# Kernel tuning notes

Measured on AMD Instinct MI355X. Metric: run time of the kernel, lower is better.

## Reference

```python
import jax, jax.numpy as jnp
import numpy as np

L, D, H, HK, DH, F, V, T, B = 8, 1024, 16, 4, 64, 2816, 32000, 1024, 2
G = H // HK
THETA = 10000.0
EPS = 1e-6
SCALE = DH ** -0.5


def _rope_tables(t, dh, theta):
    inv = 1.0 / theta ** (jnp.arange(0, dh, 2, dtype=jnp.float32) / dh)  # [dh/2]
    ang = jnp.arange(t, dtype=jnp.float32)[:, None] * inv[None, :]       # [T, dh/2]
    return jnp.cos(ang), jnp.sin(ang)


def _apply_rope(x, cos, sin):
    # x: [B, T, h, DH] -> rotate pairs (even, odd)
    xr = x.reshape(*x.shape[:-1], DH // 2, 2)
    x0, x1 = xr[..., 0], xr[..., 1]
    c = cos[None, :, None, :]
    s = sin[None, :, None, :]
    out = jnp.stack([x0 * c - x1 * s, x0 * s + x1 * c], axis=-1)
    return out.reshape(*x.shape)


def _rmsnorm(x, w):
    var = jnp.mean(x * x, axis=-1, keepdims=True)
    return x * jax.lax.rsqrt(var + EPS) * w


def setup_inputs() -> dict:
    key = jax.random.key(0)
    ks = jax.random.split(key, 10)
    s = 0.02
    return {
        "ids": jax.random.randint(ks[0], (B, T), 0, V),
        "emb": jax.random.normal(ks[1], (V, D), jnp.float32) * s,
        "qw": jax.random.normal(ks[2], (L, H * DH, D), jnp.float32) * s,
        "kw": jax.random.normal(ks[3], (L, HK * DH, D), jnp.float32) * s,
        "vw": jax.random.normal(ks[4], (L, HK * DH, D), jnp.float32) * s,
        "ow": jax.random.normal(ks[5], (L, D, D), jnp.float32) * s,
        "w1": jax.random.normal(ks[6], (L, F, D), jnp.float32) * s,
        "w2": jax.random.normal(ks[7], (L, D, F), jnp.float32) * s,
        "w3": jax.random.normal(ks[8], (L, F, D), jnp.float32) * s,
        "n1": jnp.ones((L, D), jnp.float32),
        "n2": jnp.ones((L, D), jnp.float32),
        "nf": jnp.ones((D,), jnp.float32),
    }


def _forward(ids, emb, qw, kw, vw, ow, w1, w2, w3, n1, n2, nf):
    cos, sin = _rope_tables(T, DH, THETA)
    causal = jnp.tril(jnp.ones((T, T), dtype=bool))  # [T, T]
    x = emb[ids]  # [B, T, D]
    for l in range(L):
        xn = _rmsnorm(x, n1[l])
        q = jnp.einsum("btd,ed->bte", xn, qw[l]).reshape(B, T, H, DH)
        k = jnp.einsum("btd,ed->bte", xn, kw[l]).reshape(B, T, HK, DH)
        v = jnp.einsum("btd,ed->bte", xn, vw[l]).reshape(B, T, HK, DH)
        q = _apply_rope(q, cos, sin)
        k = _apply_rope(k, cos, sin)
        # GQA: group query heads over shared kv heads
        qg = q.transpose(0, 2, 1, 3).reshape(B, HK, G, T, DH)
        kh = k.transpose(0, 2, 1, 3)  # [B, HK, T, DH]
        vh = v.transpose(0, 2, 1, 3)
        scores = jnp.einsum("bkgtd,bksd->bkgts", qg, kh) * SCALE
        scores = jnp.where(causal, scores, -jnp.inf)
        p = jax.nn.softmax(scores, axis=-1)
        out = jnp.einsum("bkgts,bksd->bkgtd", p, vh)
        out = out.reshape(B, H, T, DH).transpose(0, 2, 1, 3).reshape(B, T, D)
        x = x + jnp.einsum("btd,ed->bte", out, ow[l])
        xn2 = _rmsnorm(x, n2[l])
        h1 = jnp.einsum("btd,fd->btf", xn2, w1[l])
        h3 = jnp.einsum("btd,fd->btf", xn2, w3[l])
        x = x + jnp.einsum("btf,df->btd", jax.nn.silu(h1) * h3, w2[l])
    x = _rmsnorm(x, nf)
    logits = jnp.einsum("btd,vd->btv", x, emb)  # tied lm_head
    return logits


def reference(ids, emb, qw, kw, vw, ow, w1, w2, w3, n1, n2, nf):
    return _forward(ids, emb, qw, kw, vw, ow, w1, w2, w3, n1, n2, nf)
```

## Files before the change

kernel.cpp:

```cpp
#include <hip/hip_runtime.h>
#include <math.h>

#define L_ 8
#define D_ 1024
#define H_ 16
#define HK_ 4
#define DH_ 64
#define F_ 2816
#define V_ 32000
#define T_ 1024
#define B_ 2
#define M_ (B_*T_)
#define SCALE_ 0.125f

typedef unsigned short u16;
typedef unsigned int   u32;
typedef __attribute__((ext_vector_type(4))) float  f32x4;
typedef __attribute__((ext_vector_type(8))) short  bf16x8;
typedef __attribute__((ext_vector_type(4))) unsigned short u16x4;
typedef __attribute__((ext_vector_type(4))) unsigned int   u32x4;

__device__ __forceinline__ float bf2f(u16 h) {
    union { u32 u; float f; } v; v.u = ((u32)h) << 16; return v.f;
}
__device__ __forceinline__ u16 f2bf(float f) {
    union { float f; u32 u; } v; v.f = f;
    u32 r = v.u + 0x7fffu + ((v.u >> 16) & 1u);
    return (u16)(r >> 16);
}

__device__ __forceinline__ void gl_lds16(const void* g, void* l) {
    __builtin_amdgcn_global_load_lds(
        (const __attribute__((address_space(1))) unsigned int*)g,
        (__attribute__((address_space(3))) unsigned int*)l,
        16, 0, 0);
}

__device__ __forceinline__ void bar8() {
    asm volatile("" ::: "memory");
    __builtin_amdgcn_s_barrier();
    asm volatile("" ::: "memory");
}

template<int EPI>
__global__ __launch_bounds__(512)
void gemm8_k(const u16* __restrict__ A, int K,
             const u16* __restrict__ W, int N,
             float* __restrict__ Of, u16* __restrict__ Ob)
{
    constexpr int TS = 256 * 64;
    __shared__ u16 sA[2 * TS];
    __shared__ u16 sB[2 * TS];

    const int tid = threadIdx.x;
    const int lane = tid & 63, wv = tid >> 6;
    const int wm = wv >> 2, wn = wv & 3;
    const int l15 = lane & 15, lhi = lane >> 4;

    const int nwg = gridDim.x;
    const int q8 = nwg >> 3;
    const int xcd = blockIdx.x & 7, off8 = blockIdx.x >> 3;
    const int wgid = xcd * q8 + off8;
    const int tM = wgid & 7, tN = wgid >> 3;

    const u16* Abase = A + (size_t)(tM * 256) * K;
    const u16* Wbase = W + (size_t)(tN * 256) * K;

    const int srow8 = lane >> 3;
    const int sp    = lane & 7;
    const int scol  = (sp ^ srow8) * 8;

    auto stage = [&](const u16* gbase, int t2, int h, u16* dst) {
        const u16* g = gbase + (size_t)(h * 128) * K + (t2 << 6);
        u16* d = dst + h * 8192;
#pragma unroll
        for (int i = 0; i < 2; ++i) {
            int c = wv * 2 + i;
            int row = c * 8 + srow8;
            gl_lds16(g + (size_t)row * K + scol, d + c * 512);
        }
    };

    f32x4 acc[8][4];
#pragma unroll
    for (int i = 0; i < 8; ++i)
#pragma unroll
        for (int j = 0; j < 4; ++j) acc[i][j] = f32x4{0.f, 0.f, 0.f, 0.f};

    const int nt = K >> 6;
    stage(Abase, 0, 0, sA); stage(Abase, 0, 1, sA);
    stage(Wbase, 0, 0, sB); stage(Wbase, 0, 1, sB);
    if (nt > 1) {
        stage(Wbase, 1, 0, sB + TS); stage(Wbase, 1, 1, sB + TS);
        asm volatile("s_waitcnt vmcnt(4)" ::: "memory");
    } else {
        asm volatile("s_waitcnt vmcnt(0)" ::: "memory");
    }
    bar8();

    for (int t = 0; t < nt; ++t) {
        const int cur = t & 1;
        const u16* sa = sA + cur * TS;
        const u16* sb = sB + cur * TS;
        u16* saN = sA + (cur ^ 1) * TS;
        u16* sbN = sB + cur * TS;

        bf16x8 breg[4][2];

#pragma unroll
        for (int p = 0; p < 4; ++p) {
            if (p == 0) {
#pragma unroll
                for (int j = 0; j < 4; ++j)
#pragma unroll
                    for (int kk = 0; kk < 2; ++kk) {
                        int br = wn * 64 + j * 16 + l15;
                        int ls = kk * 4 + lhi;
                        breg[j][kk] = *(const bf16x8*)
                            &sb[br * 64 + ((ls ^ (br & 7)) * 8)];
                    }
            }
            bf16x8 areg[2][2];
#pragma unroll
            for (int mi = 0; mi < 2; ++mi)
#pragma unroll
                for (int kk = 0; kk < 2; ++kk) {
                    int ar = wm * 128 + (p * 2 + mi) * 16 + l15;
                    int ls = kk * 4 + lhi;
                    areg[mi][kk] = *(const bf16x8*)
                        &sa[ar * 64 + ((ls ^ (ar & 7)) * 8)];
                }

            if (p == 0 && t + 1 < nt) stage(Abase, t + 1, 0, saN);
            if (p == 1 && t + 1 < nt) stage(Abase, t + 1, 1, saN);
            if (p == 2 && t + 2 < nt) stage(Wbase, t + 2, 0, sbN);
            if (p == 3 && t + 2 < nt) stage(Wbase, t + 2, 1, sbN);

            if (p == 3 && t + 1 < nt) {
                if (t + 2 < nt) asm volatile("s_waitcnt vmcnt(4)" ::: "memory");
                else            asm volatile("s_waitcnt vmcnt(0)" ::: "memory");
            }

            bar8();
            asm volatile("s_waitcnt lgkmcnt(0)" ::: "memory");
            __builtin_amdgcn_s_setprio(1);
#pragma unroll
            for (int mi = 0; mi < 2; ++mi)
#pragma unroll
                for (int j = 0; j < 4; ++j)
#pragma unroll
                    for (int kk = 0; kk < 2; ++kk)
                        acc[p * 2 + mi][j] = __builtin_amdgcn_mfma_f32_16x16x32_bf16(
                            areg[mi][kk], breg[j][kk], acc[p * 2 + mi][j], 0, 0, 0);
            __builtin_amdgcn_s_setprio(0);
            bar8();
        }
    }

    if (EPI == 1) {
        float* sw = (float*)sA + wv * (16 * 68);
        const int cc = l15;
#pragma unroll
        for (int i = 0; i < 8; ++i) {
#pragma unroll
            for (int j = 0; j < 4; ++j)
#pragma unroll
                for (int r = 0; r < 4; ++r)
                    sw[(lhi * 4 + r) * 68 + j * 16 + l15] = acc[i][j][r];
#pragma unroll
            for (int g = 0; g < 4; ++g) {
                int row = g * 4 + lhi;
                f32x4 v = *(const f32x4*)&sw[row * 68 + cc * 4];
                size_t gm = (size_t)tM * 256 + wm * 128 + i * 16 + row;
                size_t gn = (size_t)tN * 256 + wn * 64 + cc * 4;
                *(f32x4*)&Of[gm * (size_t)N + gn] = v;
            }
        }
    } else {
#pragma unroll
        for (int i = 0; i < 8; ++i)
#pragma unroll
            for (int j = 0; j < 4; ++j) {
                size_t gm = (size_t)tM * 256 + wm * 128 + i * 16 + lhi * 4;
                size_t gn = (size_t)tN * 256 + wn * 64 + j * 16 + l15;
#pragma unroll
                for (int r = 0; r < 4; ++r) {
                    float v = acc[i][j][r];
                    float b = __shfl_xor(v, 1);
                    if ((lane & 1) == 0) {
                        float s = v / (1.0f + expf(-v));
                        Ob[(gm + r) * (size_t)F_ + (gn >> 1)] = f2bf(s * b);
                    }
                }
            }
    }
}

template<int BM, int BN, int EPI>
__global__ __launch_bounds__(256)
void gemm2_k(const u16* __restrict__ A, int K,
             const u16* __restrict__ W, int N,
             float* __restrict__ Of, u16* __restrict__ Ob,
             const float* __restrict__ tc, const float* __restrict__ ts)
{
    constexpr int FM = BM / 32;
    constexpr int FN = BN / 32;
    constexpr int GM = M_ / BM;
    constexpr int IPA = BM / 64;
    constexpr int IPB = BN / 64;
    __shared__ u16 sA[2 * BM * 32];
    __shared__ u16 sB[2 * BN * 32];

    const int tid  = threadIdx.x;
    const int lane = tid & 63, wv = tid >> 6;
    const int wm = wv >> 1, wn = wv & 1;
    const int l15 = lane & 15, lhi = lane >> 4;
    const int m0 = wm * (BM / 2), n0 = wn * (BN / 2);

    const int nwg = gridDim.x;
    const int q8 = nwg >> 3, r8 = nwg & 7;
    const int xcd = blockIdx.x & 7, off8 = blockIdx.x >> 3;
    const int wgid = (xcd < r8 ? xcd * (q8 + 1) : r8 * (q8 + 1) + (xcd - r8) * q8) + off8;
    const int tM = wgid % GM, tN = wgid / GM;

    const int srow = lane >> 2;
    const int scol = (lane & 3) * 8;

    const u16* Abase = A + (size_t)(tM * BM) * K;
    const u16* Wbase = W + (size_t)(tN * BN) * K;

    f32x4 acc[FM][FN];
#pragma unroll
    for (int i = 0; i < FM; ++i)
#pragma unroll
        for (int j = 0; j < FN; ++j) acc[i][j] = f32x4{0.f, 0.f, 0.f, 0.f};

    auto stage = [&](int kt, int buf) {
        u16* sa = sA + buf * (BM * 32);
        u16* sb = sB + buf * (BN * 32);
#pragma unroll
        for (int i = 0; i < IPA; ++i) {
            int c = wv * IPA + i;
            gl_lds16(Abase + (size_t)(c * 16 + srow) * K + kt + scol, sa + c * 512);
        }
#pragma unroll
        for (int i = 0; i < IPB; ++i) {
            int c = wv * IPB + i;
            gl_lds16(Wbase + (size_t)(c * 16 + srow) * K + kt + scol, sb + c * 512);
        }
    };

    const int nt = K >> 5;
    stage(0, 0);
    asm volatile("s_waitcnt vmcnt(0)" ::: "memory");
    __syncthreads();

    int cur = 0;
    for (int t = 0; t < nt; ++t) {
        if (t + 1 < nt) stage((t + 1) << 5, cur ^ 1);

        const u16* sa = sA + cur * (BM * 32);
        const u16* sb = sB + cur * (BN * 32);
        bf16x8 av[FM], bv[FN];
#pragma unroll
        for (int i = 0; i < FM; ++i)
            av[i] = *(const bf16x8*)&sa[(m0 + i * 16 + l15) * 32 + lhi * 8];
#pragma unroll
        for (int j = 0; j < FN; ++j)
            bv[j] = *(const bf16x8*)&sb[(n0 + j * 16 + l15) * 32 + lhi * 8];
#pragma unroll
        for (int i = 0; i < FM; ++i)
#pragma unroll
            for (int j = 0; j < FN; ++j)
                acc[i][j] = __builtin_amdgcn_mfma_f32_16x16x32_bf16(
                    av[i], bv[j], acc[i][j], 0, 0, 0);

        if (t + 1 < nt) {
            asm volatile("s_waitcnt vmcnt(0)" ::: "memory");
            __syncthreads();
            cur ^= 1;
        }
    }

#pragma unroll
    for (int i = 0; i < FM; ++i)
#pragma unroll
        for (int j = 0; j < FN; ++j) {
            size_t gm = (size_t)tM * BM + m0 + i * 16 + lhi * 4;
            size_t gn = (size_t)tN * BN + n0 + j * 16 + l15;
#pragma unroll
            for (int r = 0; r < 4; ++r) {
                float v = acc[i][j][r];
                size_t idx = (gm + r) * (size_t)N + gn;
                if (EPI == 0) {
                    Ob[idx] = f2bf(v);
                } else if (EPI == 1) {
                    Of[idx] = v;
                } else if (EPI == 2) {
                    Of[idx] += v;
                } else if (EPI == 3) {
                    float b = __shfl_xor(v, 1);
                    if ((lane & 1) == 0) {
                        float s = v / (1.0f + expf(-v));
                        Ob[(gm + r) * (size_t)F_ + (gn >> 1)] = f2bf(s * b);
                    }
                } else {
                    float b = __shfl_xor(v, 1);
                    int gni = (int)gn;
                    int gmr = (int)(gm + r);
                    if (gni < 1280) {
                        int dd = gni & 63;
                        int jj = dd >> 1;
                        int tt = gmr & (T_ - 1);
                        float c = tc[tt * 32 + jj], s = ts[tt * 32 + jj];
                        float ro = ((dd & 1) == 0) ? (v * c - b * s) : (b * s + v * c);
                        Ob[idx] = f2bf(ro);
                    } else {
                        int vc = gni - 1280;
                        int hk = vc >> 6, dd = vc & 63;
                        int bb = gmr >> 10, tt = gmr & (T_ - 1);
                        ((u16*)Of)[((size_t)((bb * HK_ + hk) * DH_ + dd)) * T_ + tt] = f2bf(v);
                    }
                }
            }
        }
}

__global__ __launch_bounds__(256)
void cvt_k(const float* __restrict__ src, u16* __restrict__ dst,
           unsigned long long sStride, unsigned long long dStride)
{
    int l = blockIdx.y;
    size_t i = ((size_t)blockIdx.x * 256 + threadIdx.x) * 4;
    f32x4 v = *(const f32x4*)(src + l * sStride + i);
    u16x4 o;
    o.x = f2bf(v.x); o.y = f2bf(v.y); o.z = f2bf(v.z); o.w = f2bf(v.w);
    *(u16x4*)(dst + l * dStride + i) = o;
}

__global__ __launch_bounds__(256)
void cvt_il_k(const float* __restrict__ src, u16* __restrict__ dst,
              unsigned long long sStride, unsigned long long dStride, int off)
{
    int f = blockIdx.x, l = blockIdx.y;
    int i = threadIdx.x * 4;
    f32x4 v = *(const f32x4*)(src + l * sStride + (size_t)f * D_ + i);
    u16x4 o;
    o.x = f2bf(v.x); o.y = f2bf(v.y); o.z = f2bf(v.z); o.w = f2bf(v.w);
    *(u16x4*)(dst + l * dStride + (size_t)(2 * f + off) * D_ + i) = o;
}

template<int BM, int BN, int EPI, int NW>
__global__ __launch_bounds__(256)
void gemm_k(const u16* __restrict__ A, int K,
            const float* __restrict__ W0, const float* __restrict__ W1p,
            const float* __restrict__ W2p, int N0, int N1, int N,
            float* __restrict__ Of, u16* __restrict__ Ob)
{
    constexpr int FM = BM / 32;
    constexpr int FN = BN / 32;
    constexpr int LS = 40;
    __shared__ u16 sA[BM * LS];
    __shared__ u16 sB[BN * LS];

    const int tid  = threadIdx.x;
    const int lane = tid & 63, wv = tid >> 6;
    const int wm = wv >> 1, wn = wv & 1;
    const int l15 = lane & 15, lhi = lane >> 4;
    const int m0 = wm * (BM / 2), n0 = wn * (BN / 2);
    const int tM = blockIdx.y, tN = blockIdx.x;

    f32x4 acc[FM][FN];
#pragma unroll
    for (int i = 0; i < FM; ++i)
#pragma unroll
        for (int j = 0; j < FN; ++j) acc[i][j] = f32x4{0.f, 0.f, 0.f, 0.f};

    for (int kt = 0; kt < K; kt += 32) {
#pragma unroll
        for (int i = 0; i < BM / 64; ++i) {
            int cid = tid + i * 256;
            int row = cid >> 2, kc = cid & 3;
            const u16* src = A + (size_t)(tM * BM + row) * K + kt + kc * 8;
            *(u32x4*)&sA[row * LS + kc * 8] = *(const u32x4*)src;
        }
#pragma unroll
        for (int i = 0; i < BN / 32; ++i) {
            int cid = tid + i * 256;
            int row = cid >> 3, kc = cid & 7;
            int n = tN * BN + row;
            const float* wr;
            if (NW == 1)      wr = W0 + (size_t)n * K;
            else if (NW == 2) wr = (n < N0) ? (W0 + (size_t)n * K)
                                            : (W1p + (size_t)(n - N0) * K);
            else              wr = (n < N0) ? (W0 + (size_t)n * K)
                               : (n < N0 + N1) ? (W1p + (size_t)(n - N0) * K)
                                               : (W2p + (size_t)(n - N0 - N1) * K);
            f32x4 v = *(const f32x4*)(wr + kt + kc * 4);
            u16x4 o;
            o.x = f2bf(v.x); o.y = f2bf(v.y); o.z = f2bf(v.z); o.w = f2bf(v.w);
            *(u16x4*)&sB[row * LS + kc * 4] = o;
        }
        __syncthreads();

        bf16x8 av[FM], bv[FN];
#pragma unroll
        for (int i = 0; i < FM; ++i)
            av[i] = *(const bf16x8*)&sA[(m0 + i * 16 + l15) * LS + lhi * 8];
#pragma unroll
        for (int j = 0; j < FN; ++j)
            bv[j] = *(const bf16x8*)&sB[(n0 + j * 16 + l15) * LS + lhi * 8];
#pragma unroll
        for (int i = 0; i < FM; ++i)
#pragma unroll
            for (int j = 0; j < FN; ++j)
                acc[i][j] = __builtin_amdgcn_mfma_f32_16x16x32_bf16(
                    av[i], bv[j], acc[i][j], 0, 0, 0);
        __syncthreads();
    }

#pragma unroll
    for (int i = 0; i < FM; ++i)
#pragma unroll
        for (int j = 0; j < FN; ++j) {
            size_t gm = (size_t)tM * BM + m0 + i * 16 + lhi * 4;
            size_t gn = (size_t)tN * BN + n0 + j * 16 + l15;
#pragma unroll
            for (int r = 0; r < 4; ++r) {
                float v = acc[i][j][r];
                size_t idx = (gm + r) * (size_t)N + gn;
                if (EPI == 0)      Ob[idx] = f2bf(v);
                else if (EPI == 1) Of[idx] = v;
                else               Of[idx] += v;
            }
        }
}

__global__ __launch_bounds__(512)
void attn3_k(const u16* __restrict__ qkv, const u16* __restrict__ vt,
             u16* __restrict__ attn)
{
    const int qt = 31 - blockIdx.x;
    const int hk = blockIdx.y, b = blockIdx.z;
    const int tid = threadIdx.x;
    const int lane = tid & 63, w = tid >> 6;
    const int l15 = lane & 15, lhi = lane >> 4;
    const int h = hk * 4 + (w & 3);
    const int rg = w >> 2;

    __shared__ u16 sK[128 * 64];
    __shared__ u16 sVT[64 * 128];
    __shared__ u16 sP[8][16 * 136];

    const int q0 = qt * 32;
    const int qr0 = q0 + rg * 16;
    const u16* qptr = qkv + (size_t)(b * T_ + qr0 + l15) * 1536 + h * 64 + lhi * 8;
    bf16x8 aq0 = *(const bf16x8*)qptr;
    bf16x8 aq1 = *(const bf16x8*)(qptr + 32);

    f32x4 accO[4];
#pragma unroll
    for (int d = 0; d < 4; ++d) accO[d] = f32x4{0.f, 0.f, 0.f, 0.f};
    float m_r[4] = {-1e30f, -1e30f, -1e30f, -1e30f};
    float l_r[4] = {0.f, 0.f, 0.f, 0.f};
    const int myq = qr0 + lhi * 4;
    const int qmaxw = qr0 + 15;
    u16* sPw = sP[w];

    const int ntiles = (qt >> 2) + 1;
    const u16* vtb = vt + (size_t)((b * HK_ + hk) * DH_) * T_;
    const int L = lane;

    for (int kt = 0; kt < ntiles; ++kt) {
        const int t0 = kt * 128;
#pragma unroll
        for (int i = 0; i < 2; ++i) {
            int c = w * 2 + i;
            int row = c * 8 + (L >> 3);
            int p = L & 7;
            const u16* src = qkv + (size_t)(b * T_ + t0 + row) * 1536 + 1024 + hk * 64
                             + ((p ^ (row & 7)) * 8);
            gl_lds16(src, sK + c * 512);
        }
#pragma unroll
        for (int i = 0; i < 2; ++i) {
            int c = w * 2 + i;
            int row = c * 4 + (L >> 4);
            int p = L & 15;
            const u16* src = vtb + (size_t)row * T_ + t0 + ((p ^ (row & 15)) * 8);
            gl_lds16(src, sVT + c * 512);
        }
        asm volatile("s_waitcnt vmcnt(0)" ::: "memory");
        __syncthreads();

        const bool lastt = (kt == ntiles - 1);

        f32x4 accS[8];
#pragma unroll
        for (int nf = 0; nf < 8; ++nf)
            accS[nf] = f32x4{-1e30f, -1e30f, -1e30f, -1e30f};
#pragma unroll
        for (int pk = 0; pk < 4; ++pk) {
            if (t0 + pk * 32 > qmaxw) continue;
            f32x4 s0 = f32x4{0.f, 0.f, 0.f, 0.f};
            f32x4 s1 = f32x4{0.f, 0.f, 0.f, 0.f};
#pragma unroll
            for (int kk = 0; kk < 2; ++kk) {
                bf16x8 aqs = kk ? aq1 : aq0;
                int r0 = (pk * 2) * 16 + l15;
                int r1 = (pk * 2 + 1) * 16 + l15;
                int ls = kk * 4 + lhi;
                bf16x8 b0 = *(const bf16x8*)&sK[r0 * 64 + ((ls ^ (r0 & 7)) * 8)];
                bf16x8 b1 = *(const bf16x8*)&sK[r1 * 64 + ((ls ^ (r1 & 7)) * 8)];
                s0 = __builtin_amdgcn_mfma_f32_16x16x32_bf16(aqs, b0, s0, 0, 0, 0);
                s1 = __builtin_amdgcn_mfma_f32_16x16x32_bf16(aqs, b1, s1, 0, 0, 0);
            }
#pragma unroll
            for (int r = 0; r < 4; ++r) {
                float v0 = s0[r] * SCALE_;
                float v1 = s1[r] * SCALE_;
                if (lastt) {
                    int kp0 = t0 + (pk * 2) * 16 + l15;
                    int kp1 = kp0 + 16;
                    if (kp0 > myq + r) v0 = -1e30f;
                    if (kp1 > myq + r) v1 = -1e30f;
                }
                accS[pk * 2][r] = v0;
                accS[pk * 2 + 1][r] = v1;
            }
        }

        float sc[4];
#pragma unroll
        for (int r = 0; r < 4; ++r) {
            float mx = accS[0][r];
#pragma unroll
            for (int nf = 1; nf < 8; ++nf) mx = fmaxf(mx, accS[nf][r]);
#pragma unroll
            for (int off = 1; off < 16; off <<= 1) mx = fmaxf(mx, __shfl_xor(mx, off));
            float mn = fmaxf(m_r[r], mx);
            sc[r] = expf(m_r[r] - mn);
            m_r[r] = mn;
        }
        float rs[4] = {0.f, 0.f, 0.f, 0.f};
#pragma unroll
        for (int pk = 0; pk < 4; ++pk) {
            if (t0 + pk * 32 > qmaxw) continue;
#pragma unroll
            for (int g = 0; g < 2; ++g) {
                int nf = pk * 2 + g;
#pragma unroll
                for (int r = 0; r < 4; ++r) {
                    float p = expf(accS[nf][r] - m_r[r]);
                    accS[nf][r] = p;
                    rs[r] += p;
                }
            }
        }
#pragma unroll
        for (int r = 0; r < 4; ++r) {
#pragma unroll
            for (int off = 1; off < 16; off <<= 1) rs[r] += __shfl_xor(rs[r], off);
            l_r[r] = l_r[r] * sc[r] + rs[r];
        }
#pragma unroll
        for (int d = 0; d < 4; ++d)
#pragma unroll
            for (int r = 0; r < 4; ++r) accO[d][r] *= sc[r];

#pragma unroll
        for (int pk = 0; pk < 4; ++pk) {
            if (t0 + pk * 32 > qmaxw) continue;
#pragma unroll
            for (int g = 0; g < 2; ++g) {
                int nf = pk * 2 + g;
#pragma unroll
                for (int r = 0; r < 4; ++r)
                    sPw[(lhi * 4 + r) * 136 + nf * 16 + l15] = f2bf(accS[nf][r]);
            }
        }

#pragma unroll
        for (int kk = 0; kk < 4; ++kk) {
            if (t0 + kk * 32 > qmaxw) continue;
            bf16x8 pas = *(const bf16x8*)&sPw[l15 * 136 + kk * 32 + lhi * 8];
#pragma unroll
            for (int nf = 0; nf < 4; ++nf) {
                int row = nf * 16 + l15;
                int ls = kk * 4 + lhi;
                bf16x8 bvv = *(const bf16x8*)&sVT[row * 128 + ((ls ^ (row & 15)) * 8)];
                accO[nf] = __builtin_amdgcn_mfma_f32_16x16x32_bf16(pas, bvv, accO[nf], 0, 0, 0);
            }
        }
        __syncthreads();
    }

#pragma unroll
    for (int d = 0; d < 4; ++d)
#pragma unroll
        for (int r = 0; r < 4; ++r) {
            int row = qr0 + lhi * 4 + r;
            float o = accO[d][r] / l_r[r];
            attn[(size_t)(b * T_ + row) * 1024 + h * 64 + d * 16 + l15] = f2bf(o);
        }
}

__global__ __launch_bounds__(256)
void attn_k(const u16* __restrict__ qkv, u16* __restrict__ attn)
{
    const int qt = blockIdx.x, h = blockIdx.y, b = blockIdx.z;
    const int hk = h >> 2;
    const int tid = threadIdx.x;
    const int lane = tid & 63, w = tid >> 6;
    const int l15 = lane & 15, lhi = lane >> 4;
    __shared__ u16 sK[64 * 72];
    __shared__ u16 sVT[64 * 74];
    __shared__ u16 sP[4 * 16 * 72];

    const int q0 = qt * 64;
    const u16* qptr = qkv + (size_t)(b * T_ + q0 + w * 16 + l15) * 1536 + h * 64 + lhi * 8;
    bf16x8 aq0 = *(const bf16x8*)qptr;
    bf16x8 aq1 = *(const bf16x8*)(qptr + 32);

    f32x4 accO[4];
#pragma unroll
    for (int d = 0; d < 4; ++d) accO[d] = f32x4{0.f, 0.f, 0.f, 0.f};
    float m_r[4] = {-1e30f, -1e30f, -1e30f, -1e30f};
    float l_r[4] = {0.f, 0.f, 0.f, 0.f};
    const int myq = q0 + w * 16 + lhi * 4;
    u16* sPw = sP + w * 16 * 72;

    for (int kt = 0; kt <= qt; ++kt) {
#pragma unroll
        for (int i = 0; i < 2; ++i) {
            int cid = tid + i * 256;
            int r = cid >> 3, kc = cid & 7;
            const u16* src = qkv + (size_t)(b * T_ + kt * 64 + r) * 1536 + 1024 + hk * 64 + kc * 8;
            *(u32x4*)&sK[r * 72 + kc * 8] = *(const u32x4*)src;
        }
#pragma unroll
        for (int i = 0; i < 2; ++i) {
            int cid = tid + i * 256;
            int tt = cid >> 3, dc = cid & 7;
            const u16* src = qkv + (size_t)(b * T_ + kt * 64 + tt) * 1536 + 1280 + hk * 64 + dc * 8;
            bf16x8 vv = *(const bf16x8*)src;
#pragma unroll
            for (int j = 0; j < 8; ++j) sVT[(dc * 8 + j) * 74 + tt] = (u16)vv[j];
        }
        __syncthreads();

        f32x4 accS[4];
#pragma unroll
        for (int nf = 0; nf < 4; ++nf) accS[nf] = f32x4{0.f, 0.f, 0.f, 0.f};
#pragma unroll
        for (int s = 0; s < 2; ++s) {
            bf16x8 aqs = s ? aq1 : aq0;
#pragma unroll
            for (int nf = 0; nf < 4; ++nf) {
                bf16x8 bk = *(const bf16x8*)&sK[(nf * 16 + l15) * 72 + s * 32 + lhi * 8];
                accS[nf] = __builtin_amdgcn_mfma_f32_16x16x32_bf16(aqs, bk, accS[nf], 0, 0, 0);
            }
        }
#pragma unroll
        for (int nf = 0; nf < 4; ++nf)
#pragma unroll
            for (int r = 0; r < 4; ++r) {
                float v = accS[nf][r] * SCALE_;
                if (kt == qt) {
                    int kp = kt * 64 + nf * 16 + l15;
                    if (kp > myq + r) v = -1e30f;
                }
                accS[nf][r] = v;
            }
        float sc[4];
#pragma unroll
        for (int r = 0; r < 4; ++r) {
            float mx = fmaxf(fmaxf(accS[0][r], accS[1][r]), fmaxf(accS[2][r], accS[3][r]));
#pragma unroll
            for (int off = 1; off < 16; off <<= 1) mx = fmaxf(mx, __shfl_xor(mx, off));
            float mn = fmaxf(m_r[r], mx);
            sc[r] = expf(m_r[r] - mn);
            m_r[r] = mn;
        }
        float rs[4] = {0.f, 0.f, 0.f, 0.f};
#pragma unroll
        for (int nf = 0; nf < 4; ++nf)
#pragma unroll
            for (int r = 0; r < 4; ++r) {
                float p = expf(accS[nf][r] - m_r[r]);
                accS[nf][r] = p;
                rs[r] += p;
            }
#pragma unroll
        for (int r = 0; r < 4; ++r) {
#pragma unroll
            for (int off = 1; off < 16; off <<= 1) rs[r] += __shfl_xor(rs[r], off);
            l_r[r] = l_r[r] * sc[r] + rs[r];
        }
#pragma unroll
        for (int d = 0; d < 4; ++d)
#pragma unroll
            for (int r = 0; r < 4; ++r) accO[d][r] *= sc[r];

#pragma unroll
        for (int nf = 0; nf < 4; ++nf)
#pragma unroll
            for (int r = 0; r < 4; ++r)
                sPw[(lhi * 4 + r) * 72 + nf * 16 + l15] = f2bf(accS[nf][r]);
        bf16x8 pa0 = *(const bf16x8*)&sPw[l15 * 72 + lhi * 8];
        bf16x8 pa1 = *(const bf16x8*)&sPw[l15 * 72 + 32 + lhi * 8];
#pragma unroll
        for (int s = 0; s < 2; ++s) {
            bf16x8 pas = s ? pa1 : pa0;
#pragma unroll
            for (int d = 0; d < 4; ++d) {
                bf16x8 bvv = *(const bf16x8*)&sVT[(d * 16 + l15) * 74 + s * 32 + lhi * 8];
                accO[d] = __builtin_amdgcn_mfma_f32_16x16x32_bf16(pas, bvv, accO[d], 0, 0, 0);
            }
        }
        __syncthreads();
    }

#pragma unroll
    for (int d = 0; d < 4; ++d)
#pragma unroll
        for (int r = 0; r < 4; ++r) {
            int row = q0 + w * 16 + lhi * 4 + r;
            float o = accO[d][r] / l_r[r];
            attn[(size_t)(b * T_ + row) * 1024 + h * 64 + d * 16 + l15] = f2bf(o);
        }
}

__global__ __launch_bounds__(256)
void gather_k(const int* __restrict__ ids, const float* __restrict__ emb,
              float* __restrict__ x)
{
    int m = blockIdx.x, tid = threadIdx.x;
    int id = ids[m];
    *(f32x4*)(x + (size_t)m * D_ + tid * 4) =
        *(const f32x4*)(emb + (size_t)id * D_ + tid * 4);
}

__global__ __launch_bounds__(256)
void rmsnorm_k(const float* __restrict__ x, const float* __restrict__ g,
               u16* __restrict__ out)
{
    const int row = blockIdx.x, tid = threadIdx.x;
    const float* xr = x + (size_t)row * D_;
    f32x4 v = *(const f32x4*)(xr + tid * 4);
    float ss = v.x * v.x + v.y * v.y + v.z * v.z + v.w * v.w;
#pragma unroll
    for (int off = 32; off >= 1; off >>= 1) ss += __shfl_xor(ss, off);
    __shared__ float red[4];
    if ((tid & 63) == 0) red[tid >> 6] = ss;
    __syncthreads();
    float tot = red[0] + red[1] + red[2] + red[3];
    float rr = rsqrtf(tot * (1.0f / D_) + 1e-6f);
    f32x4 wv = *(const f32x4*)(g + tid * 4);
    u16x4 o;
    o.x = f2bf(v.x * rr * wv.x); o.y = f2bf(v.y * rr * wv.y);
    o.z = f2bf(v.z * rr * wv.z); o.w = f2bf(v.w * rr * wv.w);
    *(u16x4*)(out + (size_t)row * D_ + tid * 4) = o;
}

__global__ __launch_bounds__(256)
void rope_tab_k(float* __restrict__ tc, float* __restrict__ ts)
{
    int idx = blockIdx.x * 256 + threadIdx.x;
    int t = idx >> 5, j = idx & 31;
    float inv = powf(10000.0f, -(float)j * (1.0f / 32.0f));
    float ang = (float)t * inv;
    tc[idx] = cosf(ang);
    ts[idx] = sinf(ang);
}

__global__ __launch_bounds__(256)
void silu_f32_k(const float* __restrict__ h13, u16* __restrict__ hh)
{
    int m = blockIdx.y;
    int f = blockIdx.x * 256 + threadIdx.x;
    float a = h13[(size_t)m * (2 * F_) + f];
    float c = h13[(size_t)m * (2 * F_) + F_ + f];
    float s = a / (1.0f + expf(-a));
    hh[(size_t)m * F_ + f] = f2bf(s * c);
}

__global__ __launch_bounds__(640)
void rope_slow_k(u16* __restrict__ qkv)
{
    int m = blockIdx.x;
    int c2 = threadIdx.x;
    int col = (c2 < 512) ? (c2 * 2) : (1024 + (c2 - 512) * 2);
    int d = col & 63;
    int t = m & (T_ - 1);
    float ang = (float)t * powf(10000.0f, -(float)d / 64.0f);
    float cs = cosf(ang), sn = sinf(ang);
    u16* p = qkv + (size_t)m * 1536 + col;
    float x0 = bf2f(p[0]), x1 = bf2f(p[1]);
    p[0] = f2bf(x0 * cs - x1 * sn);
    p[1] = f2bf(x0 * sn + x1 * cs);
}

extern "C" void kernel_launch(void* const* d_in, const int* in_sizes, int n_in,
                              void* d_out, int out_size, void* d_ws, size_t ws_size,
                              hipStream_t stream)
{
    const int*   ids = (const int*)d_in[0];
    const float* emb = (const float*)d_in[1];
    const float* qw  = (const float*)d_in[2];
    const float* kw  = (const float*)d_in[3];
    const float* vw  = (const float*)d_in[4];
    const float* ow  = (const float*)d_in[5];
    const float* w1  = (const float*)d_in[6];
    const float* w2  = (const float*)d_in[7];
    const float* w3  = (const float*)d_in[8];
    const float* n1  = (const float*)d_in[9];
    const float* n2  = (const float*)d_in[10];
    const float* nfw = (const float*)d_in[11];
    float* out = (float*)d_out;
    char*  ws  = (char*)d_ws;

    float* x    = (float*)(ws);
    u16*   xn   = (u16*)(ws + 8388608ULL);
    u16*   qkvb = (u16*)(ws + 12582912ULL);
    u16*   attnb= (u16*)(ws + 18874368ULL);
    u16*   hh   = (u16*)(ws + 46137344ULL);
    float* ropec= (float*)(ws + 57671680ULL);
    float* ropes= (float*)(ws + 57802752ULL);
    u16*   embb = (u16*)(ws + 57933824ULL);
    u16*   wqkv = (u16*)(ws + 123469824ULL);
    u16*   wob  = (u16*)(ws + 148635648ULL);
    u16*   w13b = (u16*)(ws + 165412864ULL);
    u16*   w2b  = (u16*)(ws + 257687552ULL);
    u16*   vtb  = (u16*)(ws + 303824896ULL);
    const unsigned long long NEED = 304873472ULL;

    if (ws_size >= NEED) {
        cvt_k<<<dim3(32000, 1), 256, 0, stream>>>(emb, embb, 0, 0);
        cvt_k<<<dim3(1024, L_), 256, 0, stream>>>(qw, wqkv,            1048576ULL, 1572864ULL);
        cvt_k<<<dim3(256,  L_), 256, 0, stream>>>(kw, wqkv + 1048576,  262144ULL,  1572864ULL);
        cvt_k<<<dim3(256,  L_), 256, 0, stream>>>(vw, wqkv + 1310720,  262144ULL,  1572864ULL);
        cvt_k<<<dim3(1024, L_), 256, 0, stream>>>(ow, wob,             1048576ULL, 1048576ULL);
        cvt_il_k<<<dim3(2816, L_), 256, 0, stream>>>(w1, w13b, 2883584ULL, 5767168ULL, 0);
        cvt_il_k<<<dim3(2816, L_), 256, 0, stream>>>(w3, w13b, 2883584ULL, 5767168ULL, 1);
        cvt_k<<<dim3(2816, L_), 256, 0, stream>>>(w2, w2b,             2883584ULL, 2883584ULL);
        rope_tab_k<<<T_ * 32 / 256, 256, 0, stream>>>(ropec, ropes);

        gather_k<<<M_, 256, 0, stream>>>(ids, emb, x);

        for (int l = 0; l < L_; ++l) {
            rmsnorm_k<<<M_, 256, 0, stream>>>(x, n1 + l * D_, xn);
            gemm2_k<64, 64, 4><<<32 * 24, 256, 0, stream>>>(
                xn, D_, wqkv + (size_t)l * 1572864, 1536, (float*)vtb, qkvb, ropec, ropes);
            attn3_k<<<dim3(32, HK_, B_), 512, 0, stream>>>(qkvb, vtb, attnb);
            gemm2_k<64, 64, 2><<<32 * 16, 256, 0, stream>>>(
                attnb, D_, wob + (size_t)l * 1048576, 1024, x, nullptr, nullptr, nullptr);
            rmsnorm_k<<<M_, 256, 0, stream>>>(x, n2 + l * D_, xn);
            gemm2_k<128, 128, 3><<<16 * 44, 256, 0, stream>>>(
                xn, D_, w13b + (size_t)l * 5767168, 5632, nullptr, hh, nullptr, nullptr);
            gemm2_k<64, 64, 2><<<32 * 16, 256, 0, stream>>>(
                hh, F_, w2b + (size_t)l * 2883584, 1024, x, nullptr, nullptr, nullptr);
        }

        rmsnorm_k<<<M_, 256, 0, stream>>>(x, nfw, xn);
        gemm8_k<1><<<8 * 125, 512, 0, stream>>>(
            xn, D_, embb, V_, out, nullptr);
        return;
    }

    float* h13f = (float*)(ws + 23068672ULL);
    u16*   hhf  = (u16*)(ws + 69206016ULL);
    gather_k<<<M_, 256, 0, stream>>>(ids, emb, x);

    for (int l = 0; l < L_; ++l) {
        rmsnorm_k<<<M_, 256, 0, stream>>>(x, n1 + l * D_, xn);
        gemm_k<128, 64, 0, 3><<<dim3(24, 16), 256, 0, stream>>>(
            xn, D_,
            qw + (size_t)l * H_ * DH_ * D_,
            kw + (size_t)l * HK_ * DH_ * D_,
            vw + (size_t)l * HK_ * DH_ * D_,
            1024, 256, 1536, nullptr, qkvb);
        rope_slow_k<<<M_, 640, 0, stream>>>(qkvb);
        attn_k<<<dim3(T_ / 64, H_, B_), 256, 0, stream>>>(qkvb, attnb);
        gemm_k<128, 64, 2, 1><<<dim3(16, 16), 256, 0, stream>>>(
            attnb, D_, ow + (size_t)l * D_ * D_, nullptr, nullptr,
            0, 0, D_, x, nullptr);
        rmsnorm_k<<<M_, 256, 0, stream>>>(x, n2 + l * D_, xn);
        gemm_k<128, 128, 1, 2><<<dim3(44, 16), 256, 0, stream>>>(
            xn, D_, w1 + (size_t)l * F_ * D_, w3 + (size_t)l * F_ * D_, nullptr,
            F_, 0, 2 * F_, h13f, nullptr);
        silu_f32_k<<<dim3(11, M_), 256, 0, stream>>>(h13f, hhf);
        gemm_k<128, 64, 2, 1><<<dim3(16, 16), 256, 0, stream>>>(
            hhf, F_, w2 + (size_t)l * D_ * F_, nullptr, nullptr,
            0, 0, D_, x, nullptr);
    }

    rmsnorm_k<<<M_, 256, 0, stream>>>(x, nfw, xn);
    gemm_k<128, 128, 1, 1><<<dim3(250, 16), 256, 0, stream>>>(
        xn, D_, emb, nullptr, nullptr, 0, 0, V_, out, nullptr);
}
```

Baseline: 1.807 ms.

## Split-K down-projection GEMM, fuse residual add into RMSNorm, merge prep kernels

The FFN down-projection GEMM (K=2816) now runs as a 2-way split-K. Each half writes its partial sum to a separate fp32 buffer, which doubles the workgroup count to improve CU occupancy. The residual add of both partials moves into a new rmsnorm_add_k, used before the next layer's attention norm and before the final norm. All weight conversions, the embedding gather and the rope table are merged into a single prep kernel to cut launch count. The cost is extra partial-buffer traffic to and from global memory.

```diff
diff --git a/kernel.cpp b/kernel.cpp
--- a/kernel.cpp
+++ b/kernel.cpp
@@ -221,13 +221,22 @@
     const int q8 = nwg >> 3, r8 = nwg & 7;
     const int xcd = blockIdx.x & 7, off8 = blockIdx.x >> 3;
     const int wgid = (xcd < r8 ? xcd * (q8 + 1) : r8 * (q8 + 1) + (xcd - r8) * q8) + off8;
-    const int tM = wgid % GM, tN = wgid / GM;
+
+    int tM, tN, kh = 0, koff = 0, Klen = K;
+    if (EPI == 5) {
+        kh = wgid & 1;
+        int wg2 = wgid >> 1;
+        tM = wg2 % GM; tN = wg2 / GM;
+        Klen = K >> 1; koff = kh * Klen;
+    } else {
+        tM = wgid % GM; tN = wgid / GM;
+    }
 
     const int srow = lane >> 2;
     const int scol = (lane & 3) * 8;
 
-    const u16* Abase = A + (size_t)(tM * BM) * K;
-    const u16* Wbase = W + (size_t)(tN * BN) * K;
+    const u16* Abase = A + (size_t)(tM * BM) * K + koff;
+    const u16* Wbase = W + (size_t)(tN * BN) * K + koff;
 
     f32x4 acc[FM][FN];
 #pragma unroll
@@ -250,7 +259,7 @@
         }
     };
 
-    const int nt = K >> 5;
+    const int nt = Klen >> 5;
     stage(0, 0);
     asm volatile("s_waitcnt vmcnt(0)" ::: "memory");
     __syncthreads();
@@ -298,6 +307,8 @@
                     Of[idx] = v;
                 } else if (EPI == 2) {
                     Of[idx] += v;
+                } else if (EPI == 5) {
+                    Of[(size_t)kh * (M_ * (size_t)D_) + idx] = v;
                 } else if (EPI == 3) {
                     float b = __shfl_xor(v, 1);
                     if ((lane & 1) == 0) {
@@ -327,27 +338,69 @@
 }
 
 __global__ __launch_bounds__(256)
-void cvt_k(const float* __restrict__ src, u16* __restrict__ dst,
-           unsigned long long sStride, unsigned long long dStride)
-{
-    int l = blockIdx.y;
-    size_t i = ((size_t)blockIdx.x * 256 + threadIdx.x) * 4;
-    f32x4 v = *(const f32x4*)(src + l * sStride + i);
+void prep_k(const float* __restrict__ emb, const float* __restrict__ qw,
+            const float* __restrict__ kw, const float* __restrict__ vw,
+            const float* __restrict__ ow, const float* __restrict__ w1,
+            const float* __restrict__ w2, const float* __restrict__ w3,
+            const int* __restrict__ ids,
+            u16* __restrict__ embb, u16* __restrict__ wqkv,
+            u16* __restrict__ wob, u16* __restrict__ w13b,
+            u16* __restrict__ w2b, float* __restrict__ x,
+            float* __restrict__ tc, float* __restrict__ ts)
+{
+    const int bx = blockIdx.x, tid = threadIdx.x;
+    const float* src = nullptr;
+    u16* dst = nullptr;
+
+    if (bx < 32000) {
+        src = emb + (size_t)bx * 1024;           dst = embb + (size_t)bx * 1024;
+    } else if (bx < 40192) {
+        int lb = bx - 32000, l = lb >> 10, j = lb & 1023;
+        src = qw + (size_t)l * 1048576 + j * 1024;
+        dst = wqkv + (size_t)l * 1572864 + j * 1024;
+    } else if (bx < 42240) {
+        int lb = bx - 40192, l = lb >> 8, j = lb & 255;
+        src = kw + (size_t)l * 262144 + j * 1024;
+        dst = wqkv + (size_t)l * 1572864 + 1048576 + j * 1024;
+    } else if (bx < 44288) {
+        int lb = bx - 42240, l = lb >> 8, j = lb & 255;
+        src = vw + (size_t)l * 262144 + j * 1024;
+        dst = wqkv + (size_t)l * 1572864 + 1310720 + j * 1024;
+    } else if (bx < 52480) {
+        int lb = bx - 44288, l = lb >> 10, j = lb & 1023;
+        src = ow + (size_t)l * 1048576 + j * 1024;
+        dst = wob + (size_t)l * 1048576 + j * 1024;
+    } else if (bx < 75008) {
+        int lb = bx - 52480, l = lb / 2816, f = lb - l * 2816;
+        src = w1 + (size_t)l * 2883584 + (size_t)f * 1024;
+        dst = w13b + (size_t)l * 5767168 + (size_t)(2 * f) * 1024;
+    } else if (bx < 97536) {
+        int lb = bx - 75008, l = lb / 2816, f = lb - l * 2816;
+        src = w3 + (size_t)l * 2883584 + (size_t)f * 1024;
+        dst = w13b + (size_t)l * 5767168 + (size_t)(2 * f + 1) * 1024;
+    } else if (bx < 120064) {
+        int lb = bx - 97536, l = lb / 2816, f = lb - l * 2816;
+        src = w2 + (size_t)l * 2883584 + (size_t)f * 1024;
+        dst = w2b + (size_t)l * 2883584 + (size_t)f * 1024;
+    } else if (bx < 122112) {
+        int m = bx - 120064;
+        int id = ids[m];
+        *(f32x4*)(x + (size_t)m * D_ + tid * 4) =
+            *(const f32x4*)(emb + (size_t)id * D_ + tid * 4);
+        return;
+    } else {
+        int idx = (bx - 122112) * 256 + tid;
+        int t = idx >> 5, j = idx & 31;
+        float inv = powf(10000.0f, -(float)j * (1.0f / 32.0f));
+        float ang = (float)t * inv;
+        tc[idx] = cosf(ang);
+        ts[idx] = sinf(ang);
+        return;
+    }
+    f32x4 v = *(const f32x4*)(src + tid * 4);
     u16x4 o;
     o.x = f2bf(v.x); o.y = f2bf(v.y); o.z = f2bf(v.z); o.w = f2bf(v.w);
-    *(u16x4*)(dst + l * dStride + i) = o;
-}
-
-__global__ __launch_bounds__(256)
-void cvt_il_k(const float* __restrict__ src, u16* __restrict__ dst,
-              unsigned long long sStride, unsigned long long dStride, int off)
-{
-    int f = blockIdx.x, l = blockIdx.y;
-    int i = threadIdx.x * 4;
-    f32x4 v = *(const f32x4*)(src + l * sStride + (size_t)f * D_ + i);
-    u16x4 o;
-    o.x = f2bf(v.x); o.y = f2bf(v.y); o.z = f2bf(v.z); o.w = f2bf(v.w);
-    *(u16x4*)(dst + l * dStride + (size_t)(2 * f + off) * D_ + i) = o;
+    *(u16x4*)(dst + tid * 4) = o;
 }
 
 template<int BM, int BN, int EPI, int NW>
@@ -764,14 +817,33 @@
 }
 
 __global__ __launch_bounds__(256)
-void rope_tab_k(float* __restrict__ tc, float* __restrict__ ts)
-{
-    int idx = blockIdx.x * 256 + threadIdx.x;
-    int t = idx >> 5, j = idx & 31;
-    float inv = powf(10000.0f, -(float)j * (1.0f / 32.0f));
-    float ang = (float)t * inv;
-    tc[idx] = cosf(ang);
-    ts[idx] = sinf(ang);
+void rmsnorm_add_k(float* __restrict__ x, const float* __restrict__ p,
+                   const float* __restrict__ g, u16* __restrict__ out)
+{
+    const int row = blockIdx.x, tid = threadIdx.x;
+    float* xr = x + (size_t)row * D_;
+    const float* p0 = p + (size_t)row * D_;
+    const float* p1 = p + (size_t)(M_ * (size_t)D_) + (size_t)row * D_;
+    f32x4 a = *(const f32x4*)(xr + tid * 4);
+    f32x4 b = *(const f32x4*)(p0 + tid * 4);
+    f32x4 c = *(const f32x4*)(p1 + tid * 4);
+    f32x4 v;
+    v.x = a.x + b.x + c.x; v.y = a.y + b.y + c.y;
+    v.z = a.z + b.z + c.z; v.w = a.w + b.w + c.w;
+    *(f32x4*)(xr + tid * 4) = v;
+    float ss = v.x * v.x + v.y * v.y + v.z * v.z + v.w * v.w;
+#pragma unroll
+    for (int off = 32; off >= 1; off >>= 1) ss += __shfl_xor(ss, off);
+    __shared__ float red[4];
+    if ((tid & 63) == 0) red[tid >> 6] = ss;
+    __syncthreads();
+    float tot = red[0] + red[1] + red[2] + red[3];
+    float rr = rsqrtf(tot * (1.0f / D_) + 1e-6f);
+    f32x4 wv = *(const f32x4*)(g + tid * 4);
+    u16x4 o;
+    o.x = f2bf(v.x * rr * wv.x); o.y = f2bf(v.y * rr * wv.y);
+    o.z = f2bf(v.z * rr * wv.z); o.w = f2bf(v.w * rr * wv.w);
+    *(u16x4*)(out + (size_t)row * D_ + tid * 4) = o;
 }
 
 __global__ __launch_bounds__(256)
@@ -824,6 +896,7 @@
     u16*   xn   = (u16*)(ws + 8388608ULL);
     u16*   qkvb = (u16*)(ws + 12582912ULL);
     u16*   attnb= (u16*)(ws + 18874368ULL);
+    float* pW   = (float*)(ws + 23068672ULL);
     u16*   hh   = (u16*)(ws + 46137344ULL);
     float* ropec= (float*)(ws + 57671680ULL);
     float* ropes= (float*)(ws + 57802752ULL);
@@ -836,20 +909,15 @@
     const unsigned long long NEED = 304873472ULL;
 
     if (ws_size >= NEED) {
-        cvt_k<<<dim3(32000, 1), 256, 0, stream>>>(emb, embb, 0, 0);
-        cvt_k<<<dim3(1024, L_), 256, 0, stream>>>(qw, wqkv,            1048576ULL, 1572864ULL);
-        cvt_k<<<dim3(256,  L_), 256, 0, stream>>>(kw, wqkv + 1048576,  262144ULL,  1572864ULL);
-        cvt_k<<<dim3(256,  L_), 256, 0, stream>>>(vw, wqkv + 1310720,  262144ULL,  1572864ULL);
-        cvt_k<<<dim3(1024, L_), 256, 0, stream>>>(ow, wob,             1048576ULL, 1048576ULL);
-        cvt_il_k<<<dim3(2816, L_), 256, 0, stream>>>(w1, w13b, 2883584ULL, 5767168ULL, 0);
-        cvt_il_k<<<dim3(2816, L_), 256, 0, stream>>>(w3, w13b, 2883584ULL, 5767168ULL, 1);
-        cvt_k<<<dim3(2816, L_), 256, 0, stream>>>(w2, w2b,             2883584ULL, 2883584ULL);
-        rope_tab_k<<<T_ * 32 / 256, 256, 0, stream>>>(ropec, ropes);
-
-        gather_k<<<M_, 256, 0, stream>>>(ids, emb, x);
+        prep_k<<<122240, 256, 0, stream>>>(
+            emb, qw, kw, vw, ow, w1, w2, w3, ids,
+            embb, wqkv, wob, w13b, w2b, x, ropec, ropes);
 
         for (int l = 0; l < L_; ++l) {
-            rmsnorm_k<<<M_, 256, 0, stream>>>(x, n1 + l * D_, xn);
+            if (l == 0)
+                rmsnorm_k<<<M_, 256, 0, stream>>>(x, n1, xn);
+            else
+                rmsnorm_add_k<<<M_, 256, 0, stream>>>(x, pW, n1 + l * D_, xn);
             gemm2_k<64, 64, 4><<<32 * 24, 256, 0, stream>>>(
                 xn, D_, wqkv + (size_t)l * 1572864, 1536, (float*)vtb, qkvb, ropec, ropes);
             attn3_k<<<dim3(32, HK_, B_), 512, 0, stream>>>(qkvb, vtb, attnb);
@@ -858,11 +926,11 @@
             rmsnorm_k<<<M_, 256, 0, stream>>>(x, n2 + l * D_, xn);
             gemm2_k<128, 128, 3><<<16 * 44, 256, 0, stream>>>(
                 xn, D_, w13b + (size_t)l * 5767168, 5632, nullptr, hh, nullptr, nullptr);
-            gemm2_k<64, 64, 2><<<32 * 16, 256, 0, stream>>>(
-                hh, F_, w2b + (size_t)l * 2883584, 1024, x, nullptr, nullptr, nullptr);
-        }
-
-        rmsnorm_k<<<M_, 256, 0, stream>>>(x, nfw, xn);
+            gemm2_k<64, 64, 5><<<2 * 32 * 16, 256, 0, stream>>>(
+                hh, F_, w2b + (size_t)l * 2883584, 1024, pW, nullptr, nullptr, nullptr);
+        }
+
+        rmsnorm_add_k<<<M_, 256, 0, stream>>>(x, pW, nfw, xn);
         gemm8_k<1><<<8 * 125, 512, 0, stream>>>(
             xn, D_, embb, V_, out, nullptr);
         return;
```

Measured after the change: 1.719 ms. 4.8% less time.
